# Optimization experiments

Hardware: AMD Instinct MI355X
Metric: run time of the kernel (lower is better)

The kernel has to match this reference:

```python
import jax, jax.numpy as jnp
import numpy as np
from jax import lax

B, T, V, E, H, K = 64, 512, 50000, 128, 256, 9


def setup_inputs() -> dict:
    key = jax.random.key(0)
    ks = jax.random.split(key, 18)
    def n(k, shape, s=0.1):
        return jax.random.normal(k, shape, dtype=jnp.float32) * s
    emb = n(ks[0], (V, E), 1.0).at[0].set(0.0)  # padding_idx=0 row zeroed
    return {
        'sentence': jax.random.randint(ks[1], (B, T), 0, V),
        'mask': jnp.ones((B, T), dtype=bool),
        'emb': emb,
        'Wih_f': n(ks[2], (4 * H, E)), 'Whh_f': n(ks[3], (4 * H, H)),
        'bih_f': n(ks[4], (4 * H,)), 'bhh_f': n(ks[5], (4 * H,)),
        'Wih_b': n(ks[6], (4 * H, E)), 'Whh_b': n(ks[7], (4 * H, H)),
        'bih_b': n(ks[8], (4 * H,)), 'bhh_b': n(ks[9], (4 * H,)),
        'Wout': n(ks[10], (K, 2 * H)), 'bout': n(ks[11], (K,)),
        'start': n(ks[12], (K,)), 'end': n(ks[13], (K,)), 'trans': n(ks[14], (K, K)),
        'h0': n(ks[15], (2, B, H), 1.0),  # torch randn init hidden, [layers*dirs,B,H]
        'c0': n(ks[16], (2, B, H), 1.0),
    }


def lstm_dir(x, Wih, Whh, bih, bhh, h0, c0, reverse):
    # x: [B,T,E]; PyTorch LSTM cell, gate order i,f,g,o
    bias = bih + bhh
    def cell(carry, xt):
        h, c = carry
        gates = xt @ Wih.T + h @ Whh.T + bias
        i, f, g, o = jnp.split(gates, 4, axis=-1)
        c = jax.nn.sigmoid(f) * c + jax.nn.sigmoid(i) * jnp.tanh(g)
        h = jax.nn.sigmoid(o) * jnp.tanh(c)
        return (h, c), h
    _, hs = lax.scan(cell, (h0, c0), x.swapaxes(0, 1), reverse=reverse)
    return hs.swapaxes(0, 1)  # [B,T,H]


def viterbi(feats, mask, start, end, trans):
    # feats: [B,T,K]; torchcrf _viterbi_decode (batch_first)
    score0 = start[None] + feats[:, 0]  # [B,K]
    def step(score, inp):
        e_t, m_t = inp  # [B,K], [B]
        br = score[:, :, None] + trans[None]        # [B,K_prev,K_next]
        nxt = jnp.max(br, axis=1) + e_t
        idx = jnp.argmax(br, axis=1)                # [B,K]
        new = jnp.where(m_t[:, None], nxt, score)
        return new, idx
    final, hist = lax.scan(step, score0,
                           (feats[:, 1:].swapaxes(0, 1), mask[:, 1:].swapaxes(0, 1)))
    final = final + end[None]
    best = jnp.max(final, -1)
    last = jnp.argmax(final, -1)  # [B]
    def back(tag, idx_t):
        prev = jnp.take_along_axis(idx_t, tag[:, None], 1)[:, 0]
        return prev, tag
    first, rest = lax.scan(back, last, hist, reverse=True)
    tags = jnp.concatenate([first[None], rest], 0).swapaxes(0, 1)  # [B,T]
    return tags.astype(jnp.int32), best


def reference(sentence, mask, emb, Wih_f, Whh_f, bih_f, bhh_f,
              Wih_b, Whh_b, bih_b, bhh_b, Wout, bout,
              start, end, trans, h0, c0):
    x = emb[sentence]  # [B,T,E]
    hf = lstm_dir(x, Wih_f, Whh_f, bih_f, bhh_f, h0[0], c0[0], False)
    hb = lstm_dir(x, Wih_b, Whh_b, bih_b, bhh_b, h0[1], c0[1], True)
    feats = jnp.concatenate([hf, hb], -1) @ Wout.T + bout  # [B,T,K]
    tags, _ = viterbi(feats, mask, start, end, trans)
    return tags
```

## Files before the change

### kernel.cpp

```cpp
#include <hip/hip_runtime.h>
#include <math.h>

#define BB 64
#define TT 512
#define EE 128
#define HH 256
#define NK 9

#define WROW 386
#define NROWS 32
#define NB 16

#define OFF_TICK  524288ULL
#define OFF_HS    528384ULL
#define OFF_FEATS (528384ULL + 134217728ULL)

__global__ void init_kernel(double* __restrict__ hx, int* __restrict__ tick,
                            const float* __restrict__ h0) {
  int gid = blockIdx.x * 256 + threadIdx.x;
  if (gid < 2 * HH * BB) {
    int d  = gid >> 14;
    int r  = gid & 16383;
    int bs = r >> 12;
    int bb = (r >> 8) & 15;
    int u  = r & 255;
    hx[(size_t)(d * 4 + bs) * 4096 + bb * 256 + u] =
        (double)h0[d * 16384 + (bs * 16 + bb) * 256 + u];
  }
  if (gid < 256) tick[gid] = 0;
}

__launch_bounds__(256, 1)
__global__ void recur_kernel(const int* __restrict__ sent, const float* __restrict__ emb,
                             const float* __restrict__ WihF, const float* __restrict__ WhhF,
                             const float* __restrict__ bihF, const float* __restrict__ bhhF,
                             const float* __restrict__ WihB, const float* __restrict__ WhhB,
                             const float* __restrict__ bihB, const float* __restrict__ bhhB,
                             const float* __restrict__ c0,
                             double* __restrict__ hx, int* __restrict__ tick,
                             double* __restrict__ hsout) {
  extern __shared__ double sm[];
  double* wl     = sm;
  double* xh     = sm + NROWS * WROW;
  double* bias_l = xh + NB * WROW;
  double* g_l    = bias_l + 32;

  const int tid = threadIdx.x;
  const int g   = blockIdx.x & 7;
  const int dir = g >> 2;
  const int bs  = g & 3;
  const int u0  = (blockIdx.x >> 3) * 8;

  const float* Wih = dir ? WihB : WihF;
  const float* Whh = dir ? WhhB : WhhF;
  const float* bih = dir ? bihB : bihF;
  const float* bhh = dir ? bhhB : bhhF;

  for (int r = 0; r < NROWS; ++r) {
    int grow = (r >> 3) * HH + u0 + (r & 7);
    int c = tid;
    wl[r * WROW + c] = (c < EE) ? (double)Wih[(size_t)grow * EE + c]
                                : (double)Whh[(size_t)grow * HH + (c - EE)];
    if (tid < EE) wl[r * WROW + 256 + tid] = (double)Whh[(size_t)grow * HH + 128 + tid];
  }
  if (tid < NROWS) {
    int grow = (tid >> 3) * HH + u0 + (tid & 7);
    bias_l[tid] = (double)bih[grow] + (double)bhh[grow];
  }
  double creg = 0.0;
  if (tid < 128) {
    int uo = tid >> 4, bb = tid & 15;
    creg = (double)c0[dir * (BB * HH) + (bs * 16 + bb) * HH + u0 + uo];
  }

  auto x_stage = [&](int tq) {
    int t2 = tid - 128;
    int bb = t2 & 15, c = t2 >> 4;
    int tok = sent[(bs * 16 + bb) * TT + tq];
    const float4* ep = (const float4*)(emb + (size_t)tok * EE + c * 16);
    double* dst = xh + bb * WROW + c * 16;
    #pragma unroll
    for (int q = 0; q < 4; ++q) {
      float4 v = ep[q];
      dst[q * 4 + 0] = (double)v.x; dst[q * 4 + 1] = (double)v.y;
      dst[q * 4 + 2] = (double)v.z; dst[q * 4 + 3] = (double)v.w;
    }
  };

  const int rr  = tid >> 4;
  const int bbf = tid & 15;
  int* cnt = tick + g * 32;

  if (tid >= 128) x_stage(dir ? TT - 1 : 0);
  __syncthreads();

  for (int i = 0; i < TT; ++i) {
    const int tq = dir ? (TT - 1 - i) : i;

    double a0 = bias_l[rr], a1 = bias_l[rr + 16];
    {
      const double2* xr = (const double2*)(xh + bbf * WROW);
      const double2* w0 = (const double2*)(wl + rr * WROW);
      const double2* w1 = (const double2*)(wl + (rr + 16) * WROW);
      #pragma unroll 8
      for (int k = 0; k < 64; ++k) {
        double2 v = xr[k], p = w0[k], q = w1[k];
        a0 += v.x * p.x; a0 += v.y * p.y;
        a1 += v.x * q.x; a1 += v.y * q.y;
      }
    }

    if (tid == 0) {
      const int tgt = 32 * i;
      while (__hip_atomic_load(cnt, __ATOMIC_RELAXED, __HIP_MEMORY_SCOPE_AGENT) < tgt) {}
    }
    __syncthreads();

    const double* hsrc = hx + (size_t)(((i & 1) * 2 + dir) * 4 + bs) * 4096;
    {
      double hr[16];
      #pragma unroll
      for (int c = 0; c < 16; ++c)
        hr[c] = __hip_atomic_load(hsrc + c * 256 + tid,
                                  __ATOMIC_RELAXED, __HIP_MEMORY_SCOPE_AGENT);
      #pragma unroll
      for (int c = 0; c < 16; ++c)
        xh[c * WROW + EE + tid] = hr[c];
    }
    __syncthreads();

    {
      const double2* xr = (const double2*)(xh + bbf * WROW);
      const double2* w0 = (const double2*)(wl + rr * WROW);
      const double2* w1 = (const double2*)(wl + (rr + 16) * WROW);
      #pragma unroll 8
      for (int k = 64; k < 192; ++k) {
        double2 v = xr[k], p = w0[k], q = w1[k];
        a0 += v.x * p.x; a0 += v.y * p.y;
        a1 += v.x * q.x; a1 += v.y * q.y;
      }
    }
    g_l[tid] = a0;
    g_l[tid + 256] = a1;
    __syncthreads();

    if (tid < 128) {
      double iv = g_l[tid], fv = g_l[128 + tid], gv = g_l[256 + tid], ov = g_l[384 + tid];
      double is = 1.0 / (1.0 + exp(-iv));
      double fs = 1.0 / (1.0 + exp(-fv));
      double gs = tanh(gv);
      double os = 1.0 / (1.0 + exp(-ov));
      creg = fs * creg + is * gs;
      double hval = os * tanh(creg);
      int uo = tid >> 4, bb = tid & 15;
      __hip_atomic_store(hx + (size_t)((((i + 1) & 1) * 2 + dir) * 4 + bs) * 4096
                            + bb * 256 + u0 + uo,
                         hval, __ATOMIC_RELAXED, __HIP_MEMORY_SCOPE_AGENT);
      hsout[((size_t)(dir * TT + tq) * HH + u0 + uo) * 64 + bs * 16 + bb] = hval;
    } else if (i + 1 < TT) {
      x_stage(dir ? (TT - 2 - i) : (i + 1));
    }
    __syncthreads();

    if (tid == 0)
      __hip_atomic_fetch_add(cnt, 1, __ATOMIC_RELAXED, __HIP_MEMORY_SCOPE_AGENT);
  }
}

__global__ void feats_kernel(const double* __restrict__ hs, const float* __restrict__ Wout,
                             const float* __restrict__ bout, double* __restrict__ feats) {
  __shared__ double wl[NK * 2 * HH];
  __shared__ double bl[NK];
  int tid = threadIdx.x, t = blockIdx.x;
  for (int idx = tid; idx < NK * 2 * HH; idx += 256) wl[idx] = (double)Wout[idx];
  if (tid < NK) bl[tid] = (double)bout[tid];
  __syncthreads();
  if (tid < 192) {
    int bb = tid & 63, kg = tid >> 6;
    double acc0 = bl[kg * 3 + 0], acc1 = bl[kg * 3 + 1], acc2 = bl[kg * 3 + 2];
    for (int d = 0; d < 2; ++d) {
      const double* hp = hs + ((size_t)(d * TT + t) * HH) * 64 + bb;
      const double* w0 = wl + (kg * 3 + 0) * 2 * HH + d * HH;
      const double* w1 = wl + (kg * 3 + 1) * 2 * HH + d * HH;
      const double* w2 = wl + (kg * 3 + 2) * 2 * HH + d * HH;
      for (int u = 0; u < HH; ++u) {
        double hv = hp[(size_t)u * 64];
        acc0 += hv * w0[u];
        acc1 += hv * w1[u];
        acc2 += hv * w2[u];
      }
    }
    double* fp = feats + ((size_t)bb * TT + t) * NK + kg * 3;
    fp[0] = acc0; fp[1] = acc1; fp[2] = acc2;
  }
}

__global__ void viterbi_kernel(const double* __restrict__ feats, const float* __restrict__ start,
                               const float* __restrict__ endv, const float* __restrict__ trans,
                               int* __restrict__ out) {
  __shared__ double sc[NK];
  __shared__ double tr[NK * NK];
  __shared__ unsigned char hist[TT - 1][16];
  __shared__ unsigned char tags[TT];
  int lane = threadIdx.x, b = blockIdx.x;
  for (int idx = lane; idx < NK * NK; idx += 64) tr[idx] = (double)trans[idx];
  const double* fb = feats + (size_t)b * TT * NK;
  if (lane < NK) sc[lane] = (double)start[lane] + fb[lane];
  __syncthreads();
  double ftn = (lane < NK) ? fb[NK + lane] : 0.0;
  for (int t = 1; t < TT; ++t) {
    double ft = ftn;
    if (t + 1 < TT && lane < NK) ftn = fb[(size_t)(t + 1) * NK + lane];
    double best = -1e300; int arg = 0;
    if (lane < NK) {
      #pragma unroll
      for (int p = 0; p < NK; ++p) {
        double v = sc[p] + tr[p * NK + lane];
        if (v > best) { best = v; arg = p; }
      }
      hist[t - 1][lane] = (unsigned char)arg;
    }
    __syncthreads();
    if (lane < NK) sc[lane] = best + ft;
    __syncthreads();
  }
  if (lane < NK) sc[lane] += (double)endv[lane];
  __syncthreads();
  if (lane == 0) {
    double best = -1e300; int tag = 0;
    for (int n = 0; n < NK; ++n) if (sc[n] > best) { best = sc[n]; tag = n; }
    tags[TT - 1] = (unsigned char)tag;
    for (int t = TT - 2; t >= 0; --t) { tag = hist[t][tag]; tags[t] = (unsigned char)tag; }
  }
  __syncthreads();
  for (int j = lane; j < TT; j += 64) out[b * TT + j] = (int)tags[j];
}

extern "C" void kernel_launch(void* const* d_in, const int* in_sizes, int n_in,
                              void* d_out, int out_size, void* d_ws, size_t ws_size,
                              hipStream_t stream) {
  const int*   sent = (const int*)  d_in[0];
  const float* emb  = (const float*)d_in[2];
  const float* WihF = (const float*)d_in[3];
  const float* WhhF = (const float*)d_in[4];
  const float* bihF = (const float*)d_in[5];
  const float* bhhF = (const float*)d_in[6];
  const float* WihB = (const float*)d_in[7];
  const float* WhhB = (const float*)d_in[8];
  const float* bihB = (const float*)d_in[9];
  const float* bhhB = (const float*)d_in[10];
  const float* Wout = (const float*)d_in[11];
  const float* bout = (const float*)d_in[12];
  const float* stv  = (const float*)d_in[13];
  const float* env  = (const float*)d_in[14];
  const float* trv  = (const float*)d_in[15];
  const float* h0   = (const float*)d_in[16];
  const float* c0   = (const float*)d_in[17];

  char* ws = (char*)d_ws;
  double* hx    = (double*)ws;
  int*    tick  = (int*)(ws + OFF_TICK);
  double* hs    = (double*)(ws + OFF_HS);
  double* feats = (double*)(ws + OFF_FEATS);
  int* out = (int*)d_out;

  hipFuncSetAttribute((const void*)recur_kernel,
                      hipFuncAttributeMaxDynamicSharedMemorySize, 163840);

  init_kernel<<<128, 256, 0, stream>>>(hx, tick, h0);
  recur_kernel<<<256, 256, 152576, stream>>>(sent, emb, WihF, WhhF, bihF, bhhF,
                                             WihB, WhhB, bihB, bhhB, c0, hx, tick, hs);
  feats_kernel<<<TT, 256, 0, stream>>>(hs, Wout, bout, feats);
  viterbi_kernel<<<BB, 64, 0, stream>>>(feats, stv, env, trv, out);
}
```

Baseline: 3.777 ms.

## Keep LSTM weights in registers and split K-dimension across threads with shared reduction

```diff
diff --git a/kernel.cpp b/kernel.cpp
--- a/kernel.cpp
+++ b/kernel.cpp
@@ -7,9 +7,8 @@
 #define HH 256
 #define NK 9
 
-#define WROW 386
-#define NROWS 32
-#define NB 16
+#define XROW 416
+#define RKS  578
 
 #define OFF_TICK  524288ULL
 #define OFF_HS    528384ULL
@@ -40,75 +39,65 @@
                              double* __restrict__ hx, int* __restrict__ tick,
                              double* __restrict__ hsout) {
   extern __shared__ double sm[];
-  double* wl     = sm;
-  double* xh     = sm + NROWS * WROW;
-  double* bias_l = xh + NB * WROW;
-  double* g_l    = bias_l + 32;
+  double* xh     = sm;
+  double* red    = sm + 16 * XROW;
+  double* bias_l = red + 16 * RKS;
 
   const int tid = threadIdx.x;
   const int g   = blockIdx.x & 7;
   const int dir = g >> 2;
   const int bs  = g & 3;
   const int u0  = (blockIdx.x >> 3) * 8;
+  const int rr  = tid & 15;
+  const int q   = tid >> 4;
 
   const float* Wih = dir ? WihB : WihF;
   const float* Whh = dir ? WhhB : WhhF;
   const float* bih = dir ? bihB : bihF;
   const float* bhh = dir ? bhhB : bhhF;
 
-  for (int r = 0; r < NROWS; ++r) {
-    int grow = (r >> 3) * HH + u0 + (r & 7);
-    int c = tid;
-    wl[r * WROW + c] = (c < EE) ? (double)Wih[(size_t)grow * EE + c]
-                                : (double)Whh[(size_t)grow * HH + (c - EE)];
-    if (tid < EE) wl[r * WROW + 256 + tid] = (double)Whh[(size_t)grow * HH + 128 + tid];
-  }
-  if (tid < NROWS) {
-    int grow = (tid >> 3) * HH + u0 + (tid & 7);
-    bias_l[tid] = (double)bih[grow] + (double)bhh[grow];
+  const size_t g0 = (size_t)((rr >> 3) * HH + u0 + (rr & 7));
+  const size_t g1 = g0 + 2 * (size_t)HH;
+  double2 wx0[4], wx1[4], wh0[8], wh1[8];
+  #pragma unroll
+  for (int j = 0; j < 4; ++j) {
+    wx0[j] = double2{(double)Wih[g0 * EE + q * 8 + 2 * j], (double)Wih[g0 * EE + q * 8 + 2 * j + 1]};
+    wx1[j] = double2{(double)Wih[g1 * EE + q * 8 + 2 * j], (double)Wih[g1 * EE + q * 8 + 2 * j + 1]};
+  }
+  #pragma unroll
+  for (int j = 0; j < 8; ++j) {
+    wh0[j] = double2{(double)Whh[g0 * HH + q * 16 + 2 * j], (double)Whh[g0 * HH + q * 16 + 2 * j + 1]};
+    wh1[j] = double2{(double)Whh[g1 * HH + q * 16 + 2 * j], (double)Whh[g1 * HH + q * 16 + 2 * j + 1]};
+  }
+  if (tid < 32) {
+    int gr = (tid >> 3) * HH + u0 + (tid & 7);
+    bias_l[tid] = (double)bih[gr] + (double)bhh[gr];
   }
   double creg = 0.0;
-  if (tid < 128) {
-    int uo = tid >> 4, bb = tid & 15;
-    creg = (double)c0[dir * (BB * HH) + (bs * 16 + bb) * HH + u0 + uo];
-  }
+  if (rr < 8)
+    creg = (double)c0[dir * (BB * HH) + (bs * 16 + q) * HH + u0 + rr];
 
   auto x_stage = [&](int tq) {
-    int t2 = tid - 128;
-    int bb = t2 & 15, c = t2 >> 4;
-    int tok = sent[(bs * 16 + bb) * TT + tq];
-    const float4* ep = (const float4*)(emb + (size_t)tok * EE + c * 16);
-    double* dst = xh + bb * WROW + c * 16;
-    #pragma unroll
-    for (int q = 0; q < 4; ++q) {
-      float4 v = ep[q];
-      dst[q * 4 + 0] = (double)v.x; dst[q * 4 + 1] = (double)v.y;
-      dst[q * 4 + 2] = (double)v.z; dst[q * 4 + 3] = (double)v.w;
+    int rank = q * 8 + (rr - 8);
+    int bb_s = rank >> 3, cp = rank & 7;
+    int tok = sent[(bs * 16 + bb_s) * TT + tq];
+    const float4* ep = (const float4*)(emb + (size_t)tok * EE + cp * 16);
+    double* dst = xh + bb_s * XROW + cp * 16;
+    #pragma unroll
+    for (int m = 0; m < 4; ++m) {
+      float4 v = ep[m];
+      dst[m * 4 + 0] = (double)v.x; dst[m * 4 + 1] = (double)v.y;
+      dst[m * 4 + 2] = (double)v.z; dst[m * 4 + 3] = (double)v.w;
     }
   };
 
-  const int rr  = tid >> 4;
-  const int bbf = tid & 15;
   int* cnt = tick + g * 32;
 
-  if (tid >= 128) x_stage(dir ? TT - 1 : 0);
+  if (rr >= 8) x_stage(dir ? TT - 1 : 0);
   __syncthreads();
 
   for (int i = 0; i < TT; ++i) {
     const int tq = dir ? (TT - 1 - i) : i;
-
-    double a0 = bias_l[rr], a1 = bias_l[rr + 16];
-    {
-      const double2* xr = (const double2*)(xh + bbf * WROW);
-      const double2* w0 = (const double2*)(wl + rr * WROW);
-      const double2* w1 = (const double2*)(wl + (rr + 16) * WROW);
-      #pragma unroll 8
-      for (int k = 0; k < 64; ++k) {
-        double2 v = xr[k], p = w0[k], q = w1[k];
-        a0 += v.x * p.x; a0 += v.y * p.y;
-        a1 += v.x * q.x; a1 += v.y * q.y;
-      }
-    }
 
     if (tid == 0) {
       const int tgt = 32 * i;
@@ -117,46 +106,72 @@
     __syncthreads();
 
     const double* hsrc = hx + (size_t)(((i & 1) * 2 + dir) * 4 + bs) * 4096;
-    {
-      double hr[16];
+    double hr[16];
+    #pragma unroll
+    for (int c = 0; c < 16; ++c)
+      hr[c] = __hip_atomic_load(hsrc + c * 256 + tid,
+                                __ATOMIC_RELAXED, __HIP_MEMORY_SCOPE_AGENT);
+
+    double hp0[16], hp1[16];
+    #pragma unroll
+    for (int bb = 0; bb < 16; ++bb) {
+      const double2* xr = (const double2*)(xh + bb * XROW + q * 8);
+      double s0 = 0.0, s1 = 0.0;
       #pragma unroll
-      for (int c = 0; c < 16; ++c)
-        hr[c] = __hip_atomic_load(hsrc + c * 256 + tid,
-                                  __ATOMIC_RELAXED, __HIP_MEMORY_SCOPE_AGENT);
+      for (int j = 0; j < 4; ++j) {
+        double2 v = xr[j];
+        s0 += v.x * wx0[j].x; s0 += v.y * wx0[j].y;
+        s1 += v.x * wx1[j].x; s1 += v.y * wx1[j].y;
+      }
+      hp0[bb] = s0; hp1[bb] = s1;
+    }
+
+    #pragma unroll
+    for (int c = 0; c < 16; ++c)
+      xh[c * XROW + 128 + tid + 2 * (tid >> 4)] = hr[c];
+    __syncthreads();
+
+    #pragma unroll
+    for (int bb = 0; bb < 16; ++bb) {
+      const double2* hv = (const double2*)(xh + bb * XROW + 128 + 18 * q);
+      double s0 = hp0[bb], s1 = hp1[bb];
       #pragma unroll
-      for (int c = 0; c < 16; ++c)
-        xh[c * WROW + EE + tid] = hr[c];
-    }
-    __syncthreads();
-
-    {
-      const double2* xr = (const double2*)(xh + bbf * WROW);
-      const double2* w0 = (const double2*)(wl + rr * WROW);
-      const double2* w1 = (const double2*)(wl + (rr + 16) * WROW);
-      #pragma unroll 8
-      for (int k = 64; k < 192; ++k) {
-        double2 v = xr[k], p = w0[k], q = w1[k];
-        a0 += v.x * p.x; a0 += v.y * p.y;
-        a1 += v.x * q.x; a1 += v.y * q.y;
-      }
-    }
-    g_l[tid] = a0;
-    g_l[tid + 256] = a1;
-    __syncthreads();
-
-    if (tid < 128) {
-      double iv = g_l[tid], fv = g_l[128 + tid], gv = g_l[256 + tid], ov = g_l[384 + tid];
+      for (int j = 0; j < 8; ++j) {
+        double2 v = hv[j];
+        s0 += v.x * wh0[j].x; s0 += v.y * wh0[j].y;
+        s1 += v.x * wh1[j].x; s1 += v.y * wh1[j].y;
+      }
+      hp0[bb] = s0; hp1[bb] = s1;
+    }
+
+    #pragma unroll
+    for (int p = 0; p < 8; ++p) {
+      *(double2*)(red + q * RKS + rr * 18 + 2 * p)        = double2{hp0[2 * p], hp0[2 * p + 1]};
+      *(double2*)(red + q * RKS + (rr + 16) * 18 + 2 * p) = double2{hp1[2 * p], hp1[2 * p + 1]};
+    }
+    __syncthreads();
+
+    double su0 = bias_l[rr], su1 = bias_l[rr + 16];
+    #pragma unroll
+    for (int kk = 0; kk < 16; ++kk) {
+      su0 += red[kk * RKS + rr * 18 + q];
+      su1 += red[kk * RKS + (rr + 16) * 18 + q];
+    }
+    double p0 = __shfl_xor(su0, 8, 64);
+    double p1 = __shfl_xor(su1, 8, 64);
+
+    double hval = 0.0;
+    if (rr < 8) {
+      double iv = su0, gv = su1, fv = p0, ov = p1;
       double is = 1.0 / (1.0 + exp(-iv));
       double fs = 1.0 / (1.0 + exp(-fv));
       double gs = tanh(gv);
       double os = 1.0 / (1.0 + exp(-ov));
       creg = fs * creg + is * gs;
-      double hval = os * tanh(creg);
-      int uo = tid >> 4, bb = tid & 15;
+      hval = os * tanh(creg);
       __hip_atomic_store(hx + (size_t)((((i + 1) & 1) * 2 + dir) * 4 + bs) * 4096
-                            + bb * 256 + u0 + uo,
+                            + q * 256 + u0 + rr,
                          hval, __ATOMIC_RELAXED, __HIP_MEMORY_SCOPE_AGENT);
-      hsout[((size_t)(dir * TT + tq) * HH + u0 + uo) * 64 + bs * 16 + bb] = hval;
     } else if (i + 1 < TT) {
       x_stage(dir ? (TT - 2 - i) : (i + 1));
     }
@@ -164,6 +179,9 @@
 
     if (tid == 0)
       __hip_atomic_fetch_add(cnt, 1, __ATOMIC_RELAXED, __HIP_MEMORY_SCOPE_AGENT);
+
+    if (rr < 8)
+      hsout[((size_t)(dir * TT + tq) * HH + u0 + rr) * 64 + bs * 16 + q] = hval;
   }
 }
 
@@ -265,10 +283,10 @@
   int* out = (int*)d_out;
 
   hipFuncSetAttribute((const void*)recur_kernel,
-                      hipFuncAttributeMaxDynamicSharedMemorySize, 163840);
+                      hipFuncAttributeMaxDynamicSharedMemorySize, 131072);
 
   init_kernel<<<128, 256, 0, stream>>>(hx, tick, h0);
-  recur_kernel<<<256, 256, 152576, stream>>>(sent, emb, WihF, WhhF, bihF, bhhF,
+  recur_kernel<<<256, 256, 127488, stream>>>(sent, emb, WihF, WhhF, bihF, bhhF,
                                              WihB, WhhB, bihB, bhhB, c0, hx, tick, hs);
   feats_kernel<<<TT, 256, 0, stream>>>(hs, Wout, bout, feats);
   viterbi_kernel<<<BB, 64, 0, stream>>>(feats, stv, env, trv, out);
```

Result: slower. 4.029 ms (+6.7%).
